# Kernel optimization log

Hardware: AMD Instinct MI355X
Metric: run time of the kernel (lower is better)

## Reference

```python
import jax, jax.numpy as jnp
import numpy as np

ED = 1024   # encoder_dim
GH = 1024   # gnn_hidden
NL = 3      # gnn_layers
NH = 8      # gnn_heads
HD = GH // NH
N = 2048    # graph nodes
B = 1024    # query/doc batch
TEMP = 0.05
LAPW = 0.1

def _layernorm(x, g, b):
    mu = jnp.mean(x, axis=-1, keepdims=True)
    var = jnp.mean((x - mu) ** 2, axis=-1, keepdims=True)
    return (x - mu) * jax.lax.rsqrt(var + 1e-5) * g + b

def _mlp_proj(x, W1, b1, g, beta, W2, b2):
    h = _layernorm(x @ W1 + b1, g, beta)
    h = jax.nn.gelu(h, approximate=False)
    return h @ W2 + b2

def _l2norm(x):
    n = jnp.linalg.norm(x, axis=-1, keepdims=True)
    return x / jnp.maximum(n, 1e-12)

def _gnn(x, adj, gatW, a1, a2, ln_g, ln_b, poW, pob):
    mask = adj > 0
    for l in range(NL):
        Wh = jnp.einsum('nf,hfo->hno', x, gatW[l])            # [H,N,HD]
        # a([Wh_i, Wh_j]) == Wh_i@a1 + Wh_j@a2 (linear, no bias): avoids NxNx2F concat
        s1 = jnp.einsum('hno,ho->hn', Wh, a1[l])
        s2 = jnp.einsum('hno,ho->hn', Wh, a2[l])
        e = jax.nn.leaky_relu(s1[:, :, None] + s2[:, None, :], 0.2)  # [H,N,N]
        att = jax.nn.softmax(jnp.where(mask[None], e, -9e15), axis=-1)
        h = jnp.einsum('hnm,hmo->hno', att, Wh)               # [H,N,HD]
        h = jnp.transpose(h, (1, 0, 2)).reshape(x.shape[0], GH)  # concat heads
        h = jax.nn.elu(_layernorm(h, ln_g[l], ln_b[l]))
        x = x + h  # in_features == hidden so residual applies every layer
    return x @ poW + pob

def _forward(query_embeds, pos_doc_embeds, node_embeds, adj, laplacian, params):
    (qW1, qb1, qg, qbt, qW2, qb2,
     dW1, db1, dg, dbt, dW2, db2,
     gatW, a1, a2, ln_g, ln_b, poW, pob) = params
    graph_embeds = _gnn(node_embeds, adj, gatW, a1, a2, ln_g, ln_b, poW, pob)
    q = _l2norm(_mlp_proj(query_embeds, qW1, qb1, qg, qbt, qW2, qb2))
    p = _l2norm(_mlp_proj(pos_doc_embeds, dW1, db1, dg, dbt, dW2, db2))
    pos_sim = jnp.sum(q * p, axis=-1) / TEMP                  # [B]
    neg_sim = (q @ p.T) / TEMP                                # [B,B]
    logits = jnp.concatenate([pos_sim[:, None], neg_sim], axis=1)
    info_nce = jnp.mean(jax.nn.logsumexp(logits, axis=-1) - logits[:, 0])
    lap = jnp.sum(graph_embeds * (laplacian @ graph_embeds)) / graph_embeds.shape[0]
    return info_nce + LAPW * lap, info_nce, lap

def setup_inputs() -> dict:
    key = jax.random.key(0)
    ks = jax.random.split(key, 24)
    r = lambda k, s: jax.random.normal(k, s, jnp.float32) * 0.02
    adj = (jax.random.uniform(ks[3], (N, N)) < 0.02).astype(jnp.float32)
    adj = jnp.maximum(adj, jnp.eye(N, dtype=jnp.float32))
    return {
        'query_embeds': jax.random.normal(ks[0], (B, ED), jnp.float32),
        'pos_doc_embeds': jax.random.normal(ks[1], (B, ED), jnp.float32),
        'node_embeds': jax.random.normal(ks[2], (N, ED), jnp.float32),
        'adj': adj,
        'laplacian': r(ks[4], (N, N)),
        'qW1': r(ks[5], (ED, ED)), 'qb1': jnp.zeros((ED,), jnp.float32),
        'qg': jnp.ones((ED,), jnp.float32), 'qbt': jnp.zeros((ED,), jnp.float32),
        'qW2': r(ks[6], (ED, ED)), 'qb2': jnp.zeros((ED,), jnp.float32),
        'dW1': r(ks[7], (ED, ED)), 'db1': jnp.zeros((ED,), jnp.float32),
        'dg': jnp.ones((ED,), jnp.float32), 'dbt': jnp.zeros((ED,), jnp.float32),
        'dW2': r(ks[8], (ED, ED)), 'db2': jnp.zeros((ED,), jnp.float32),
        'gatW': r(ks[9], (NL, NH, ED, HD)),
        'a1': r(ks[10], (NL, NH, HD)),
        'a2': r(ks[11], (NL, NH, HD)),
        'ln_g': jnp.ones((NL, GH), jnp.float32),
        'ln_b': jnp.zeros((NL, GH), jnp.float32),
        'poW': r(ks[12], (GH, ED)),
        'pob': jnp.zeros((ED,), jnp.float32),
    }

def reference(query_embeds, pos_doc_embeds, node_embeds, adj, laplacian,
              qW1, qb1, qg, qbt, qW2, qb2,
              dW1, db1, dg, dbt, dW2, db2,
              gatW, a1, a2, ln_g, ln_b, poW, pob):
    params = (qW1, qb1, qg, qbt, qW2, qb2,
              dW1, db1, dg, dbt, dW2, db2,
              gatW, a1, a2, ln_g, ln_b, poW, pob)
    return _forward(query_embeds, pos_doc_embeds, node_embeds, adj, laplacian, params)
```

## Files before the change

kernel.cpp:

```cpp
#include <hip/hip_runtime.h>
#include <math.h>

#define ED    1024
#define GH    1024
#define NLAY  3
#define NHEAD 8
#define HD    128
#define NNODE 2048
#define BQ    1024
#define CAP   192

typedef unsigned short u16;
typedef __attribute__((ext_vector_type(8))) short short8;
typedef __attribute__((ext_vector_type(4))) float f32x4;

static const size_t OFF_X    = 0;
static const size_t OFF_XB   = 2097152;
static const size_t OFF_WHB  = 3145728;
static const size_t OFF_WTG  = 4194304;
static const size_t OFF_WTPO = 5767168;
static const size_t OFF_WTQ1 = 6291456;
static const size_t OFF_WTD1 = 6815744;
static const size_t OFF_WTQ2 = 7340032;
static const size_t OFF_WTD2 = 7864320;
static const size_t OFF_G    = 8388608;
static const size_t OFF_GT   = 10485760;
static const size_t OFF_QPB  = 11534336;
static const size_t OFF_HF   = 12582912;
static const size_t OFF_HB   = 14680064;
static const size_t OFF_FF   = 15728640;
static const size_t OFF_FB   = 17825792;
static const size_t OFF_NEG  = 18874368;
static const size_t OFF_SV1  = 19922944;
static const size_t OFF_SV2  = 19939328;
static const size_t OFF_ACC  = 19955712;
static const size_t OFF_NCNT = 19955720;
static const size_t OFF_NBR  = 19957768;

__device__ __forceinline__ u16 f2bf(float f) {
  unsigned int u = __float_as_uint(f);
  return (u16)((u + 0x7fffu + ((u >> 16) & 1u)) >> 16);
}
__device__ __forceinline__ float bf2f(u16 u) {
  return __uint_as_float(((unsigned int)u) << 16);
}

__device__ __forceinline__ float waveSum(float v) {
#pragma unroll
  for (int off = 32; off; off >>= 1) v += __shfl_xor(v, off, 64);
  return v;
}
__device__ __forceinline__ float waveMax(float v) {
#pragma unroll
  for (int off = 32; off; off >>= 1) v = fmaxf(v, __shfl_xor(v, off, 64));
  return v;
}
__device__ __forceinline__ float blockSum(float v) {
  __shared__ float buf[4];
  int lane = threadIdx.x & 63, wid = threadIdx.x >> 6, nw = (blockDim.x + 63) >> 6;
  v = waveSum(v);
  __syncthreads();
  if (lane == 0) buf[wid] = v;
  __syncthreads();
  float r = buf[0];
  for (int i = 1; i < nw; ++i) r += buf[i];
  return r;
}
__device__ __forceinline__ float blockMax(float v) {
  __shared__ float buf[4];
  int lane = threadIdx.x & 63, wid = threadIdx.x >> 6, nw = (blockDim.x + 63) >> 6;
  v = waveMax(v);
  __syncthreads();
  if (lane == 0) buf[wid] = v;
  __syncthreads();
  float r = buf[0];
  for (int i = 1; i < nw; ++i) r = fmaxf(r, buf[i]);
  return r;
}

__global__ __launch_bounds__(256) void gemm128(
    const u16* __restrict__ A, const u16* __restrict__ B0,
    const u16* __restrict__ B1, float* __restrict__ C, u16* __restrict__ Cb,
    u16* __restrict__ Ct,
    const float* __restrict__ bias0, const float* __restrict__ bias1,
    int M, int N, int K, int split, float scale) {
  __shared__ u16 As[2][128][32];
  __shared__ u16 Bs[2][128][32];
  const int tid = threadIdx.x, wave = tid >> 6, lane = tid & 63;
  const int bm = blockIdx.y * 128, bn = blockIdx.x * 128;
  const u16* Bt = (bm < split) ? B0 : B1;
  const float* bias = (bm < split) ? bias0 : bias1;

  const int sr = tid >> 2, ss = tid & 3;
  const u16* ga0 = A  + (size_t)(bm + sr) * K + ss * 8;
  const u16* ga1 = A  + (size_t)(bm + sr + 64) * K + ss * 8;
  const u16* gb0 = Bt + (size_t)(bn + sr) * K + ss * 8;
  const u16* gb1 = Bt + (size_t)(bn + sr + 64) * K + ss * 8;

  const int r16 = lane & 15, kg = lane >> 4;
  const int wm = (wave >> 1) * 64, wn = (wave & 1) * 64;

  f32x4 acc[4][4] = {};
  const int nk = K >> 5;

  float4 pa0 = *(const float4*)ga0;
  float4 pa1 = *(const float4*)ga1;
  float4 pb0 = *(const float4*)gb0;
  float4 pb1 = *(const float4*)gb1;

  for (int kt = 0; kt < nk; ++kt) {
    const int p = kt & 1;
    *(float4*)&As[p][sr][ss * 8]      = pa0;
    *(float4*)&As[p][sr + 64][ss * 8] = pa1;
    *(float4*)&Bs[p][sr][ss * 8]      = pb0;
    *(float4*)&Bs[p][sr + 64][ss * 8] = pb1;
    __syncthreads();
    if (kt + 1 < nk) {
      ga0 += 32; ga1 += 32; gb0 += 32; gb1 += 32;
      pa0 = *(const float4*)ga0;
      pa1 = *(const float4*)ga1;
      pb0 = *(const float4*)gb0;
      pb1 = *(const float4*)gb1;
    }
    short8 av[4], bv[4];
#pragma unroll
    for (int i = 0; i < 4; ++i)
      av[i] = *(const short8*)&As[p][wm + i * 16 + r16][kg * 8];
#pragma unroll
    for (int j = 0; j < 4; ++j)
      bv[j] = *(const short8*)&Bs[p][wn + j * 16 + r16][kg * 8];
#pragma unroll
    for (int i = 0; i < 4; ++i)
#pragma unroll
      for (int j = 0; j < 4; ++j)
        acc[i][j] = __builtin_amdgcn_mfma_f32_16x16x32_bf16(av[i], bv[j], acc[i][j], 0, 0, 0);
  }

  if (C) {
#pragma unroll
    for (int j = 0; j < 4; ++j) {
      int col = bn + wn + j * 16 + r16;
      float bvv = bias ? bias[col] : 0.f;
#pragma unroll
      for (int i = 0; i < 4; ++i) {
        int row0 = bm + wm + i * 16 + kg * 4;
        float* cp = C + (size_t)row0 * N + col;
#pragma unroll
        for (int r = 0; r < 4; ++r)
          cp[(size_t)r * N] = acc[i][j][r] * scale + bvv;
      }
    }
  }
  if (Cb) {
#pragma unroll
    for (int j = 0; j < 4; ++j) {
      int col = bn + wn + j * 16 + r16;
      float bvv = bias ? bias[col] : 0.f;
#pragma unroll
      for (int i = 0; i < 4; ++i) {
        int row0 = bm + wm + i * 16 + kg * 4;
        u16* cp = Cb + (size_t)row0 * N + col;
#pragma unroll
        for (int r = 0; r < 4; ++r)
          cp[(size_t)r * N] = f2bf(acc[i][j][r] * scale + bvv);
      }
    }
  }
  if (Ct) {
#pragma unroll
    for (int j = 0; j < 4; ++j) {
      int col = bn + wn + j * 16 + r16;
      float bvv = bias ? bias[col] : 0.f;
#pragma unroll
      for (int i = 0; i < 4; ++i) {
        int row0 = bm + wm + i * 16 + kg * 4;
        ushort4 o;
        o.x = f2bf(acc[i][j][0] * scale + bvv);
        o.y = f2bf(acc[i][j][1] * scale + bvv);
        o.z = f2bf(acc[i][j][2] * scale + bvv);
        o.w = f2bf(acc[i][j][3] * scale + bvv);
        *(ushort4*)&Ct[(size_t)col * M + row0] = o;
      }
    }
  }
}

__global__ __launch_bounds__(256) void gemm_dual(
    const u16* __restrict__ A0, const u16* __restrict__ B00,
    const u16* __restrict__ B01, float* __restrict__ C0, u16* __restrict__ D0,
    const float* __restrict__ e0, const float* __restrict__ f0, int M0, int sp0, float sc0,
    const float* __restrict__ A1v, const float* __restrict__ A2v,
    float* __restrict__ S1o, float* __restrict__ S2o,
    const u16* __restrict__ A1, const u16* __restrict__ B10,
    const u16* __restrict__ B11, float* __restrict__ C1, u16* __restrict__ D1,
    const float* __restrict__ e1, const float* __restrict__ f1, int M1, int sp1, float sc1) {
  const int z = blockIdx.z;
  const u16* A   = z ? A1 : A0;
  const u16* Bt0 = z ? B10 : B00;
  const u16* Bt1 = z ? B11 : B01;
  float* C = z ? C1 : C0;
  u16*   D = z ? D1 : D0;
  const float* bias0 = z ? e1 : e0;
  const float* bias1 = z ? f1 : f0;
  const int M = z ? M1 : M0, split = z ? sp1 : sp0;
  const float scale = z ? sc1 : sc0;
  const int bm = blockIdx.y * 128, bn = blockIdx.x * 128;
  if (bm >= M) return;
  const int N = 1024, K = 1024;
  const u16* Bt = (bm < split) ? Bt0 : Bt1;
  const float* bias = (bm < split) ? bias0 : bias1;

  __shared__ u16 As[2][128][32];
  __shared__ u16 Bs[2][128][32];
  const int tid = threadIdx.x, wave = tid >> 6, lane = tid & 63;
  const int sr = tid >> 2, ss = tid & 3;
  const u16* ga0 = A  + (size_t)(bm + sr) * K + ss * 8;
  const u16* ga1 = A  + (size_t)(bm + sr + 64) * K + ss * 8;
  const u16* gb0 = Bt + (size_t)(bn + sr) * K + ss * 8;
  const u16* gb1 = Bt + (size_t)(bn + sr + 64) * K + ss * 8;
  const int r16 = lane & 15, kg = lane >> 4;
  const int wm = (wave >> 1) * 64, wn = (wave & 1) * 64;

  f32x4 acc[4][4] = {};
  const int nk = 32;

  float4 pa0 = *(const float4*)ga0;
  float4 pa1 = *(const float4*)ga1;
  float4 pb0 = *(const float4*)gb0;
  float4 pb1 = *(const float4*)gb1;

  for (int kt = 0; kt < nk; ++kt) {
    const int p = kt & 1;
    *(float4*)&As[p][sr][ss * 8]      = pa0;
    *(float4*)&As[p][sr + 64][ss * 8] = pa1;
    *(float4*)&Bs[p][sr][ss * 8]      = pb0;
    *(float4*)&Bs[p][sr + 64][ss * 8] = pb1;
    __syncthreads();
    if (kt + 1 < nk) {
      ga0 += 32; ga1 += 32; gb0 += 32; gb1 += 32;
      pa0 = *(const float4*)ga0;
      pa1 = *(const float4*)ga1;
      pb0 = *(const float4*)gb0;
      pb1 = *(const float4*)gb1;
    }
    short8 av[4], bv[4];
#pragma unroll
    for (int i = 0; i < 4; ++i)
      av[i] = *(const short8*)&As[p][wm + i * 16 + r16][kg * 8];
#pragma unroll
    for (int j = 0; j < 4; ++j)
      bv[j] = *(const short8*)&Bs[p][wn + j * 16 + r16][kg * 8];
#pragma unroll
    for (int i = 0; i < 4; ++i)
#pragma unroll
      for (int j = 0; j < 4; ++j)
        acc[i][j] = __builtin_amdgcn_mfma_f32_16x16x32_bf16(av[i], bv[j], acc[i][j], 0, 0, 0);
  }

  if (C) {
#pragma unroll
    for (int j = 0; j < 4; ++j) {
      int col = bn + wn + j * 16 + r16;
      float bvv = bias ? bias[col] : 0.f;
#pragma unroll
      for (int i = 0; i < 4; ++i) {
        int row0 = bm + wm + i * 16 + kg * 4;
        float* cp = C + (size_t)row0 * N + col;
#pragma unroll
        for (int r = 0; r < 4; ++r)
          cp[(size_t)r * N] = acc[i][j][r] * scale + bvv;
      }
    }
  }
  if (D) {
#pragma unroll
    for (int j = 0; j < 4; ++j) {
      int col = bn + wn + j * 16 + r16;
      float bvv = bias ? bias[col] : 0.f;
#pragma unroll
      for (int i = 0; i < 4; ++i) {
        int row0 = bm + wm + i * 16 + kg * 4;
        u16* cp = D + (size_t)row0 * N + col;
#pragma unroll
        for (int r = 0; r < 4; ++r)
          cp[(size_t)r * N] = f2bf(acc[i][j][r] * scale + bvv);
      }
    }
  }

  if (z == 0 && S1o) {
    float c1[4], c2[4];
#pragma unroll
    for (int j = 0; j < 4; ++j) {
      int col = bn + wn + j * 16 + r16;
      c1[j] = A1v[col]; c2[j] = A2v[col];
    }
    float r1[4][4], r2[4][4];
#pragma unroll
    for (int i = 0; i < 4; ++i)
#pragma unroll
      for (int r = 0; r < 4; ++r) {
        float v1 = 0.f, v2 = 0.f;
#pragma unroll
        for (int j = 0; j < 4; ++j) {
          v1 += acc[i][j][r] * c1[j];
          v2 += acc[i][j][r] * c2[j];
        }
#pragma unroll
        for (int off = 8; off; off >>= 1) {
          v1 += __shfl_xor(v1, off, 64);
          v2 += __shfl_xor(v2, off, 64);
        }
        r1[i][r] = v1; r2[i][r] = v2;
      }
    __syncthreads();
    float* sb1 = (float*)&As[0][0][0];
    float* sb2 = sb1 + 256;
    if (r16 == 0) {
      int half = wn >> 6;
#pragma unroll
      for (int i = 0; i < 4; ++i)
#pragma unroll
        for (int r = 0; r < 4; ++r) {
          int row = wm + i * 16 + kg * 4 + r;
          sb1[half * 128 + row] = r1[i][r];
          sb2[half * 128 + row] = r2[i][r];
        }
    }
    __syncthreads();
    if (tid < 128) {
      int h = blockIdx.x;
      S1o[(h << 11) + bm + tid] = sb1[tid] + sb1[128 + tid];
      S2o[(h << 11) + bm + tid] = sb2[tid] + sb2[128 + tid];
    }
  }
}

__global__ __launch_bounds__(256) void lap_gemm(
    const float* __restrict__ A, const u16* __restrict__ Bt,
    const float* __restrict__ G, float* __restrict__ acc_out) {
  __shared__ u16 As[2][128][32];
  __shared__ u16 Bs[2][128][32];
  const int tid = threadIdx.x, wave = tid >> 6, lane = tid & 63;
  const int n = blockIdx.x;
  const int member = n >> 6, gzy = n & 63;
  const int bm = (gzy & 15) * 128, bn = member * 128, k0 = (gzy >> 4) * 512;

  const int sr = tid >> 2, ss = tid & 3;
  const float* gA0 = A + (size_t)(bm + sr) * NNODE + k0 + ss * 8;
  const float* gA1 = gA0 + (size_t)64 * NNODE;
  const u16* gb0 = Bt + (size_t)(bn + sr) * NNODE + k0 + ss * 8;
  const u16* gb1 = Bt + (size_t)(bn + sr + 64) * NNODE + k0 + ss * 8;

  const int r16 = lane & 15, kg = lane >> 4;
  const int wm = (wave >> 1) * 64, wn = (wave & 1) * 64;

  f32x4 acc[4][4] = {};
  const int nk = 16;

  float4 a0l = *(const float4*)gA0, a0h = *(const float4*)(gA0 + 4);
  float4 a1l = *(const float4*)gA1, a1h = *(const float4*)(gA1 + 4);
  float4 pb0 = *(const float4*)gb0;
  float4 pb1 = *(const float4*)gb1;

  for (int kt = 0; kt < nk; ++kt) {
    const int p = kt & 1;
    {
      ushort4 lo, hi;
      lo.x = f2bf(a0l.x); lo.y = f2bf(a0l.y); lo.z = f2bf(a0l.z); lo.w = f2bf(a0l.w);
      hi.x = f2bf(a0h.x); hi.y = f2bf(a0h.y); hi.z = f2bf(a0h.z); hi.w = f2bf(a0h.w);
      *(ushort4*)&As[p][sr][ss * 8]     = lo;
      *(ushort4*)&As[p][sr][ss * 8 + 4] = hi;
      lo.x = f2bf(a1l.x); lo.y = f2bf(a1l.y); lo.z = f2bf(a1l.z); lo.w = f2bf(a1l.w);
      hi.x = f2bf(a1h.x); hi.y = f2bf(a1h.y); hi.z = f2bf(a1h.z); hi.w = f2bf(a1h.w);
      *(ushort4*)&As[p][sr + 64][ss * 8]     = lo;
      *(ushort4*)&As[p][sr + 64][ss * 8 + 4] = hi;
    }
    *(float4*)&Bs[p][sr][ss * 8]      = pb0;
    *(float4*)&Bs[p][sr + 64][ss * 8] = pb1;
    __syncthreads();
    if (kt + 1 < nk) {
      gA0 += 32; gA1 += 32; gb0 += 32; gb1 += 32;
      a0l = *(const float4*)gA0; a0h = *(const float4*)(gA0 + 4);
      a1l = *(const float4*)gA1; a1h = *(const float4*)(gA1 + 4);
      pb0 = *(const float4*)gb0;
      pb1 = *(const float4*)gb1;
    }
    short8 av[4], bv[4];
#pragma unroll
    for (int i = 0; i < 4; ++i)
      av[i] = *(const short8*)&As[p][wm + i * 16 + r16][kg * 8];
#pragma unroll
    for (int j = 0; j < 4; ++j)
      bv[j] = *(const short8*)&Bs[p][wn + j * 16 + r16][kg * 8];
#pragma unroll
    for (int i = 0; i < 4; ++i)
#pragma unroll
      for (int j = 0; j < 4; ++j)
        acc[i][j] = __builtin_amdgcn_mfma_f32_16x16x32_bf16(av[i], bv[j], acc[i][j], 0, 0, 0);
  }

  float sum = 0.f;
#pragma unroll
  for (int j = 0; j < 4; ++j) {
    int col = bn + wn + j * 16 + r16;
#pragma unroll
    for (int i = 0; i < 4; ++i) {
      int row0 = bm + wm + i * 16 + kg * 4;
      const float* gp = G + (size_t)row0 * ED + col;
#pragma unroll
      for (int r = 0; r < 4; ++r)
        sum += acc[i][j][r] * gp[(size_t)r * ED];
    }
  }
  sum = blockSum(sum);
  if (tid == 0) atomicAdd(acc_out, sum);
}

__global__ __launch_bounds__(256) void fused_att(
    const u16* __restrict__ WHb, const float* __restrict__ S1,
    const float* __restrict__ S2, const int* __restrict__ nbr,
    const int* __restrict__ ncnt, float* __restrict__ X, u16* __restrict__ Xb,
    const float* __restrict__ g, const float* __restrict__ b) {
  __shared__ int snb[CAP];
  __shared__ float pw[NHEAD][CAP];
  const int n = blockIdx.x, t = threadIdx.x;
  const int h = t >> 5, l = t & 31;
  const int cnt = ncnt[n];
  const int cntP = (cnt + 7) & ~7;
  for (int j = t; j < cnt; j += 256) snb[j] = nbr[n * CAP + j];
  __syncthreads();
  for (int j = cnt + t; j < cntP; j += 256) snb[j] = snb[0];

  const float s1v = S1[(h << 11) + n];
  float ev[6];
  float lmax = -1e30f;
  int ne = 0;
  for (int j = l; j < cnt; j += 32) {
    float e = s1v + S2[(h << 11) + snb[j]];
    e = e > 0.f ? e : 0.2f * e;
    ev[ne++] = e;
    lmax = fmaxf(lmax, e);
  }
#pragma unroll
  for (int off = 16; off; off >>= 1) lmax = fmaxf(lmax, __shfl_xor(lmax, off, 64));
  float lsum = 0.f;
  ne = 0;
  for (int j = l; j < cnt; j += 32) {
    float p = __expf(ev[ne++] - lmax);
    pw[h][j] = p;
    lsum += p;
  }
  for (int j = cnt + l; j < cntP; j += 32) pw[h][j] = 0.f;
#pragma unroll
  for (int off = 16; off; off >>= 1) lsum += __shfl_xor(lsum, off, 64);
  const float inv = 1.f / lsum;
  __syncthreads();

  float o0 = 0.f, o1 = 0.f, o2 = 0.f, o3 = 0.f;
  const u16* wp = WHb + (t << 2);
  for (int j0 = 0; j0 < cntP; j0 += 8) {
    ushort4 buf[8];
#pragma unroll
    for (int u = 0; u < 8; ++u)
      buf[u] = *(const ushort4*)(wp + ((size_t)snb[j0 + u] << 10));
#pragma unroll
    for (int u = 0; u < 8; ++u) {
      float w = pw[h][j0 + u];
      o0 += w * bf2f(buf[u].x);
      o1 += w * bf2f(buf[u].y);
      o2 += w * bf2f(buf[u].z);
      o3 += w * bf2f(buf[u].w);
    }
  }
  o0 *= inv; o1 *= inv; o2 *= inv; o3 *= inv;

  float s  = o0 + o1 + o2 + o3;
  float sq = o0 * o0 + o1 * o1 + o2 * o2 + o3 * o3;
  float mean = blockSum(s) * (1.f / 1024.f);
  float var  = blockSum(sq) * (1.f / 1024.f) - mean * mean;
  float rstd = rsqrtf(fmaxf(var, 0.f) + 1e-5f);
  float4 xv = *(float4*)&X[((size_t)n << 10) + (t << 2)];
  float ov[4] = {o0, o1, o2, o3};
  float xa[4] = {xv.x, xv.y, xv.z, xv.w};
#pragma unroll
  for (int i = 0; i < 4; ++i) {
    int c = (t << 2) + i;
    float y = (ov[i] - mean) * rstd * g[c] + b[c];
    y = y > 0.f ? y : expm1f(y);
    xa[i] += y;
  }
  *(float4*)&X[((size_t)n << 10) + (t << 2)] = make_float4(xa[0], xa[1], xa[2], xa[3]);
  ushort4 o;
  o.x = f2bf(xa[0]); o.y = f2bf(xa[1]); o.z = f2bf(xa[2]); o.w = f2bf(xa[3]);
  *(ushort4*)&Xb[((size_t)n << 10) + (t << 2)] = o;
}

__global__ void build_nbr(const float* __restrict__ adj, int* __restrict__ nbr,
                          int* __restrict__ ncnt, float* __restrict__ acc) {
  __shared__ int cnt;
  int n = blockIdx.x, tid = threadIdx.x;
  if (n == 0 && tid < 2) acc[tid] = 0.f;
  if (tid == 0) cnt = 0;
  __syncthreads();
  for (int c = tid; c < NNODE; c += 256) {
    if (adj[((size_t)n << 11) + c] > 0.f) {
      int p = atomicAdd(&cnt, 1);
      if (p < CAP) nbr[n * CAP + p] = c;
    }
  }
  __syncthreads();
  if (tid == 0) ncnt[n] = cnt < CAP ? cnt : CAP;
}

__global__ __launch_bounds__(256) void cvt_dual(const float* __restrict__ in,
                                                float* __restrict__ Xf,
                                                u16* __restrict__ Xb) {
  int i = blockIdx.x * 256 + threadIdx.x;
  float4 v = ((const float4*)in)[i];
  ((float4*)Xf)[i] = v;
  ushort4 o;
  o.x = f2bf(v.x); o.y = f2bf(v.y); o.z = f2bf(v.z); o.w = f2bf(v.w);
  ((ushort4*)Xb)[i] = o;
}

__global__ __launch_bounds__(256) void qd_cvt(const float* __restrict__ q,
                                              const float* __restrict__ d,
                                              u16* __restrict__ out) {
  int i = blockIdx.x * 256 + threadIdx.x;
  const int half = BQ * ED / 4;
  const float* src = (i < half) ? q : d;
  int j = (i < half) ? i : i - half;
  float4 v = ((const float4*)src)[j];
  ushort4 o;
  o.x = f2bf(v.x); o.y = f2bf(v.y); o.z = f2bf(v.z); o.w = f2bf(v.w);
  ((ushort4*)out)[i] = o;
}

__device__ __forceinline__ void cvt_tr_body(const float* ip, u16* op, int R, int C) {
  __shared__ float T[64][65];
  int r0 = blockIdx.y * 64, c0 = blockIdx.x * 64;
  int t = threadIdx.x;
#pragma unroll
  for (int p = 0; p < 4; ++p) {
    int row = p * 16 + (t >> 4), col = (t & 15) * 4;
    float4 v = *(const float4*)&ip[(size_t)(r0 + row) * C + c0 + col];
    T[row][col] = v.x; T[row][col + 1] = v.y;
    T[row][col + 2] = v.z; T[row][col + 3] = v.w;
  }
  __syncthreads();
#pragma unroll
  for (int p = 0; p < 4; ++p) {
    int c = p * 16 + (t >> 4), r = (t & 15) * 4;
    ushort4 o;
    o.x = f2bf(T[r][c]); o.y = f2bf(T[r + 1][c]);
    o.z = f2bf(T[r + 2][c]); o.w = f2bf(T[r + 3][c]);
    *(ushort4*)&op[(size_t)(c0 + c) * R + r0 + r] = o;
  }
}

__global__ __launch_bounds__(256) void cvt_transpose(
    const float* __restrict__ in, u16* __restrict__ out,
    int R, int C, long inb, long outb) {
  cvt_tr_body(in + (size_t)blockIdx.z * inb, out + (size_t)blockIdx.z * outb, R, C);
}

__global__ __launch_bounds__(256) void cvt_transpose5(
    const float* __restrict__ i0, u16* __restrict__ o0,
    const float* __restrict__ i1, u16* __restrict__ o1,
    const float* __restrict__ i2, u16* __restrict__ o2,
    const float* __restrict__ i3, u16* __restrict__ o3,
    const float* __restrict__ i4, u16* __restrict__ o4) {
  const float* in; u16* out;
  switch (blockIdx.z) {
    case 0: in = i0; out = o0; break;
    case 1: in = i1; out = o1; break;
    case 2: in = i2; out = o2; break;
    case 3: in = i3; out = o3; break;
    default: in = i4; out = o4; break;
  }
  cvt_tr_body(in, out, 1024, 1024);
}

__global__ __launch_bounds__(256) void ln_gelu(
    const float* __restrict__ IN, u16* __restrict__ OUT,
    const float* __restrict__ g0, const float* __restrict__ b0,
    const float* __restrict__ g1, const float* __restrict__ b1) {
  int row = blockIdx.x, tid = threadIdx.x;
  const float* g = (row < 1024) ? g0 : g1;
  const float* b = (row < 1024) ? b0 : b1;
  float4 v = *(const float4*)&IN[((size_t)row << 10) + (tid << 2)];
  float s = v.x + v.y + v.z + v.w;
  float sq = v.x * v.x + v.y * v.y + v.z * v.z + v.w * v.w;
  float mean = blockSum(s) * (1.f / 1024.f);
  float var = blockSum(sq) * (1.f / 1024.f) - mean * mean;
  float rstd = rsqrtf(fmaxf(var, 0.f) + 1e-5f);
  float vals[4] = {v.x, v.y, v.z, v.w};
  ushort4 o;
  u16* oa = (u16*)&o;
#pragma unroll
  for (int i = 0; i < 4; ++i) {
    int c = (tid << 2) + i;
    float y = (vals[i] - mean) * rstd * g[c] + b[c];
    y = 0.5f * y * (1.f + erff(y * 0.70710678118654752f));
    oa[i] = f2bf(y);
  }
  *(ushort4*)&OUT[((size_t)row << 10) + (tid << 2)] = o;
}

__global__ __launch_bounds__(256) void l2norm_k(const float* __restrict__ IN,
                                                u16* __restrict__ OUT) {
  int row = blockIdx.x, tid = threadIdx.x;
  float4 v = *(const float4*)&IN[((size_t)row << 10) + (tid << 2)];
  float sq = v.x * v.x + v.y * v.y + v.z * v.z + v.w * v.w;
  float s = blockSum(sq);
  float inv = 1.f / fmaxf(sqrtf(s), 1e-12f);
  ushort4 o;
  o.x = f2bf(v.x * inv); o.y = f2bf(v.y * inv);
  o.z = f2bf(v.z * inv); o.w = f2bf(v.w * inv);
  *(ushort4*)&OUT[((size_t)row << 10) + (tid << 2)] = o;
}

__global__ __launch_bounds__(256) void lse_kernel(const float* __restrict__ NEG,
                                                  float* __restrict__ acc) {
  int bq = blockIdx.x, tid = threadIdx.x;
  const float* row = NEG + ((size_t)bq << 10);
  float4 v = *(const float4*)&row[tid << 2];
  float lm = fmaxf(fmaxf(v.x, v.y), fmaxf(v.z, v.w));
  float m = blockMax(lm);
  float ls = __expf(v.x - m) + __expf(v.y - m) + __expf(v.z - m) + __expf(v.w - m);
  float ssum = blockSum(ls);
  if (tid == 0) {
    float pos = row[bq];
    float loss = m + logf(ssum + __expf(pos - m)) - pos;
    atomicAdd(acc + 1, loss);
  }
}

__global__ void final_kernel(const float* __restrict__ acc, float* __restrict__ out) {
  float lap = acc[0] / 2048.f;
  float info = acc[1] / 1024.f;
  out[0] = info + 0.1f * lap;
  out[1] = info;
  out[2] = lap;
}

extern "C" void kernel_launch(void* const* d_in, const int* in_sizes, int n_in,
                              void* d_out, int out_size, void* d_ws, size_t ws_size,
                              hipStream_t stream) {
  const float* query = (const float*)d_in[0];
  const float* docs  = (const float*)d_in[1];
  const float* nodes = (const float*)d_in[2];
  const float* adj   = (const float*)d_in[3];
  const float* lapl  = (const float*)d_in[4];
  const float* qW1 = (const float*)d_in[5],  *qb1 = (const float*)d_in[6];
  const float* qg  = (const float*)d_in[7],  *qbt = (const float*)d_in[8];
  const float* qW2 = (const float*)d_in[9],  *qb2 = (const float*)d_in[10];
  const float* dW1 = (const float*)d_in[11], *db1 = (const float*)d_in[12];
  const float* dg  = (const float*)d_in[13], *dbt = (const float*)d_in[14];
  const float* dW2 = (const float*)d_in[15], *db2 = (const float*)d_in[16];
  const float* gatW = (const float*)d_in[17];
  const float* a1   = (const float*)d_in[18];
  const float* a2   = (const float*)d_in[19];
  const float* ln_g = (const float*)d_in[20];
  const float* ln_b = (const float*)d_in[21];
  const float* poW  = (const float*)d_in[22];
  const float* pob  = (const float*)d_in[23];
  float* out = (float*)d_out;

  float* ws = (float*)d_ws;
  float* X    = ws + OFF_X;
  u16*   Xb   = (u16*)(ws + OFF_XB);
  u16*   WHb  = (u16*)(ws + OFF_WHB);
  u16*   WtG  = (u16*)(ws + OFF_WTG);
  u16*   WtPO = (u16*)(ws + OFF_WTPO);
  u16*   WtQ1 = (u16*)(ws + OFF_WTQ1);
  u16*   WtD1 = (u16*)(ws + OFF_WTD1);
  u16*   WtQ2 = (u16*)(ws + OFF_WTQ2);
  u16*   WtD2 = (u16*)(ws + OFF_WTD2);
  float* G    = ws + OFF_G;
  u16*   Gt   = (u16*)(ws + OFF_GT);
  u16*   QPb  = (u16*)(ws + OFF_QPB);
  float* Hf   = ws + OFF_HF;
  u16*   Hb   = (u16*)(ws + OFF_HB);
  float* Ff   = ws + OFF_FF;
  u16*   Fb   = (u16*)(ws + OFF_FB);
  float* NEG  = ws + OFF_NEG;
  float* S1v  = ws + OFF_SV1;
  float* S2v  = ws + OFF_SV2;
  float* ACC  = ws + OFF_ACC;
  int*   NCNT = (int*)(ws + OFF_NCNT);
  int*   NBR  = (int*)(ws + OFF_NBR);

  const size_t WSL = (size_t)GH * ED;

  build_nbr<<<NNODE, 256, 0, stream>>>(adj, NBR, NCNT, ACC);
  cvt_dual<<<2048, 256, 0, stream>>>(nodes, X, Xb);
  qd_cvt<<<2048, 256, 0, stream>>>(query, docs, QPb);
  cvt_transpose<<<dim3(2, 16, 24), 256, 0, stream>>>(
      gatW, WtG, ED, HD, (long)ED * HD, (long)HD * ED);
  cvt_transpose5<<<dim3(16, 16, 5), 256, 0, stream>>>(
      poW, WtPO, qW1, WtQ1, dW1, WtD1, qW2, WtQ2, dW2, WtD2);

  gemm_dual<<<dim3(8, 16, 2), 256, 0, stream>>>(
      Xb, WtG, WtG, nullptr, WHb, nullptr, nullptr, NNODE, NNODE, 1.f,
      a1, a2, S1v, S2v,
      QPb, WtQ1, WtD1, Hf, nullptr, qb1, db1, 2 * BQ, BQ, 1.f);
  fused_att<<<NNODE, 256, 0, stream>>>(WHb, S1v, S2v, NBR, NCNT, X, Xb, ln_g, ln_b);
  ln_gelu<<<2 * BQ, 256, 0, stream>>>(Hf, Hb, qg, qbt, dg, dbt);

  gemm_dual<<<dim3(8, 16, 2), 256, 0, stream>>>(
      Xb, WtG + WSL, WtG + WSL, nullptr, WHb, nullptr, nullptr, NNODE, NNODE, 1.f,
      a1 + NHEAD * HD, a2 + NHEAD * HD, S1v, S2v,
      Hb, WtQ2, WtD2, Ff, nullptr, qb2, db2, 2 * BQ, BQ, 1.f);
  fused_att<<<NNODE, 256, 0, stream>>>(WHb, S1v, S2v, NBR, NCNT, X, Xb,
      ln_g + GH, ln_b + GH);
  l2norm_k<<<2 * BQ, 256, 0, stream>>>(Ff, Fb);

  gemm_dual<<<dim3(8, 16, 2), 256, 0, stream>>>(
      Xb, WtG + 2 * WSL, WtG + 2 * WSL, nullptr, WHb, nullptr, nullptr, NNODE, NNODE, 1.f,
      a1 + 2 * NHEAD * HD, a2 + 2 * NHEAD * HD, S1v, S2v,
      Fb, Fb + (size_t)BQ * ED, Fb + (size_t)BQ * ED, NEG, nullptr,
      nullptr, nullptr, BQ, BQ, 20.f);
  fused_att<<<NNODE, 256, 0, stream>>>(WHb, S1v, S2v, NBR, NCNT, X, Xb,
      ln_g + 2 * GH, ln_b + 2 * GH);
  lse_kernel<<<BQ, 256, 0, stream>>>(NEG, ACC);

  gemm128<<<dim3(ED / 128, NNODE / 128), 256, 0, stream>>>(
      Xb, WtPO, WtPO, G, nullptr, Gt, pob, pob, NNODE, ED, GH, NNODE, 1.f);
  lap_gemm<<<512, 256, 0, stream>>>(lapl, Gt, G, ACC);

  final_kernel<<<1, 1, 0, stream>>>(ACC, out);
}
```

Baseline: 381.8 us.

## Merge small kernels into fused launches and finalize in last lap_gemm block

Combines the three prep kernels into one grid, folds ln_gelu, l2norm and logsumexp work into the attention kernel as extra blocks, and drops the final kernel by letting the last lap_gemm block write outputs via an atomic counter. lap_gemm split-K is doubled (1024 blocks, K=256 each), the attention gather unroll goes from 8 to 16, and the A-tile store is widened to one 16-byte write. The aim is fewer launches and better overlap between independent small ops, at the cost of more atomics and register pressure.

After: 386.2 us. About the same (+1.1%).

```diff
diff --git a/kernel.cpp b/kernel.cpp
--- a/kernel.cpp
+++ b/kernel.cpp
@@ -9,6 +9,7 @@
 #define NNODE 2048
 #define BQ    1024
 #define CAP   192
+#define CAPP  208
 
 typedef unsigned short u16;
 typedef __attribute__((ext_vector_type(8))) short short8;
@@ -34,6 +35,7 @@
 static const size_t OFF_SV1  = 19922944;
 static const size_t OFF_SV2  = 19939328;
 static const size_t OFF_ACC  = 19955712;
+static const size_t OFF_CNT  = 19955714;
 static const size_t OFF_NCNT = 19955720;
 static const size_t OFF_NBR  = 19957768;
 
@@ -338,13 +340,14 @@
 
 __global__ __launch_bounds__(256) void lap_gemm(
     const float* __restrict__ A, const u16* __restrict__ Bt,
-    const float* __restrict__ G, float* __restrict__ acc_out) {
+    const float* __restrict__ G, float* __restrict__ acc,
+    int* __restrict__ cnt_done, float* __restrict__ out) {
   __shared__ u16 As[2][128][32];
   __shared__ u16 Bs[2][128][32];
   const int tid = threadIdx.x, wave = tid >> 6, lane = tid & 63;
   const int n = blockIdx.x;
-  const int member = n >> 6, gzy = n & 63;
-  const int bm = (gzy & 15) * 128, bn = member * 128, k0 = (gzy >> 4) * 512;
+  const int bn = (n >> 7) * 128, strip = n & 127;
+  const int bm = (strip & 15) * 128, k0 = (strip >> 4) * 256;
 
   const int sr = tid >> 2, ss = tid & 3;
   const float* gA0 = A + (size_t)(bm + sr) * NNODE + k0 + ss * 8;
@@ -355,8 +358,8 @@
   const int r16 = lane & 15, kg = lane >> 4;
   const int wm = (wave >> 1) * 64, wn = (wave & 1) * 64;
 
-  f32x4 acc[4][4] = {};
-  const int nk = 16;
+  f32x4 acc_r[4][4] = {};
+  const int nk = 8;
 
   float4 a0l = *(const float4*)gA0, a0h = *(const float4*)(gA0 + 4);
   float4 a1l = *(const float4*)gA1, a1h = *(const float4*)(gA1 + 4);
@@ -366,15 +369,17 @@
   for (int kt = 0; kt < nk; ++kt) {
     const int p = kt & 1;
     {
-      ushort4 lo, hi;
-      lo.x = f2bf(a0l.x); lo.y = f2bf(a0l.y); lo.z = f2bf(a0l.z); lo.w = f2bf(a0l.w);
-      hi.x = f2bf(a0h.x); hi.y = f2bf(a0h.y); hi.z = f2bf(a0h.z); hi.w = f2bf(a0h.w);
-      *(ushort4*)&As[p][sr][ss * 8]     = lo;
-      *(ushort4*)&As[p][sr][ss * 8 + 4] = hi;
-      lo.x = f2bf(a1l.x); lo.y = f2bf(a1l.y); lo.z = f2bf(a1l.z); lo.w = f2bf(a1l.w);
-      hi.x = f2bf(a1h.x); hi.y = f2bf(a1h.y); hi.z = f2bf(a1h.z); hi.w = f2bf(a1h.w);
-      *(ushort4*)&As[p][sr + 64][ss * 8]     = lo;
-      *(ushort4*)&As[p][sr + 64][ss * 8 + 4] = hi;
+      union { short8 v; ushort4 u4[2]; } w;
+      w.u4[0].x = f2bf(a0l.x); w.u4[0].y = f2bf(a0l.y);
+      w.u4[0].z = f2bf(a0l.z); w.u4[0].w = f2bf(a0l.w);
+      w.u4[1].x = f2bf(a0h.x); w.u4[1].y = f2bf(a0h.y);
+      w.u4[1].z = f2bf(a0h.z); w.u4[1].w = f2bf(a0h.w);
+      *(short8*)&As[p][sr][ss * 8] = w.v;
+      w.u4[0].x = f2bf(a1l.x); w.u4[0].y = f2bf(a1l.y);
+      w.u4[0].z = f2bf(a1l.z); w.u4[0].w = f2bf(a1l.w);
+      w.u4[1].x = f2bf(a1h.x); w.u4[1].y = f2bf(a1h.y);
+      w.u4[1].z = f2bf(a1h.z); w.u4[1].w = f2bf(a1h.w);
+      *(short8*)&As[p][sr + 64][ss * 8] = w.v;
     }
     *(float4*)&Bs[p][sr][ss * 8]      = pb0;
     *(float4*)&Bs[p][sr + 64][ss * 8] = pb1;
@@ -397,7 +402,7 @@
     for (int i = 0; i < 4; ++i)
 #pragma unroll
       for (int j = 0; j < 4; ++j)
-        acc[i][j] = __builtin_amdgcn_mfma_f32_16x16x32_bf16(av[i], bv[j], acc[i][j], 0, 0, 0);
+        acc_r[i][j] = __builtin_amdgcn_mfma_f32_16x16x32_bf16(av[i], bv[j], acc_r[i][j], 0, 0, 0);
   }
 
   float sum = 0.f;
@@ -410,131 +415,191 @@
       const float* gp = G + (size_t)row0 * ED + col;
 #pragma unroll
       for (int r = 0; r < 4; ++r)
-        sum += acc[i][j][r] * gp[(size_t)r * ED];
+        sum += acc_r[i][j][r] * gp[(size_t)r * ED];
     }
   }
   sum = blockSum(sum);
-  if (tid == 0) atomicAdd(acc_out, sum);
-}
-
-__global__ __launch_bounds__(256) void fused_att(
+  if (tid == 0) {
+    atomicAdd(acc, sum);
+    __threadfence();
+    int prev = atomicAdd(cnt_done, 1);
+    if (prev == (int)gridDim.x - 1) {
+      float lap  = atomicAdd(acc, 0.f) / 2048.f;
+      float info = atomicAdd(acc + 1, 0.f) / 1024.f;
+      out[0] = info + 0.1f * lap;
+      out[1] = info;
+      out[2] = lap;
+    }
+  }
+}
+
+__global__ __launch_bounds__(256) void att_elem(
     const u16* __restrict__ WHb, const float* __restrict__ S1,
     const float* __restrict__ S2, const int* __restrict__ nbr,
     const int* __restrict__ ncnt, float* __restrict__ X, u16* __restrict__ Xb,
-    const float* __restrict__ g, const float* __restrict__ b) {
-  __shared__ int snb[CAP];
-  __shared__ float pw[NHEAD][CAP];
-  const int n = blockIdx.x, t = threadIdx.x;
-  const int h = t >> 5, l = t & 31;
-  const int cnt = ncnt[n];
-  const int cntP = (cnt + 7) & ~7;
-  for (int j = t; j < cnt; j += 256) snb[j] = nbr[n * CAP + j];
-  __syncthreads();
-  for (int j = cnt + t; j < cntP; j += 256) snb[j] = snb[0];
-
-  const float s1v = S1[(h << 11) + n];
-  float ev[6];
-  float lmax = -1e30f;
-  int ne = 0;
-  for (int j = l; j < cnt; j += 32) {
-    float e = s1v + S2[(h << 11) + snb[j]];
-    e = e > 0.f ? e : 0.2f * e;
-    ev[ne++] = e;
-    lmax = fmaxf(lmax, e);
-  }
-#pragma unroll
-  for (int off = 16; off; off >>= 1) lmax = fmaxf(lmax, __shfl_xor(lmax, off, 64));
-  float lsum = 0.f;
-  ne = 0;
-  for (int j = l; j < cnt; j += 32) {
-    float p = __expf(ev[ne++] - lmax);
-    pw[h][j] = p;
-    lsum += p;
-  }
-  for (int j = cnt + l; j < cntP; j += 32) pw[h][j] = 0.f;
-#pragma unroll
-  for (int off = 16; off; off >>= 1) lsum += __shfl_xor(lsum, off, 64);
-  const float inv = 1.f / lsum;
-  __syncthreads();
-
-  float o0 = 0.f, o1 = 0.f, o2 = 0.f, o3 = 0.f;
-  const u16* wp = WHb + (t << 2);
-  for (int j0 = 0; j0 < cntP; j0 += 8) {
-    ushort4 buf[8];
-#pragma unroll
-    for (int u = 0; u < 8; ++u)
-      buf[u] = *(const ushort4*)(wp + ((size_t)snb[j0 + u] << 10));
-#pragma unroll
-    for (int u = 0; u < 8; ++u) {
-      float w = pw[h][j0 + u];
-      o0 += w * bf2f(buf[u].x);
-      o1 += w * bf2f(buf[u].y);
-      o2 += w * bf2f(buf[u].z);
-      o3 += w * bf2f(buf[u].w);
-    }
-  }
-  o0 *= inv; o1 *= inv; o2 *= inv; o3 *= inv;
-
-  float s  = o0 + o1 + o2 + o3;
-  float sq = o0 * o0 + o1 * o1 + o2 * o2 + o3 * o3;
-  float mean = blockSum(s) * (1.f / 1024.f);
-  float var  = blockSum(sq) * (1.f / 1024.f) - mean * mean;
-  float rstd = rsqrtf(fmaxf(var, 0.f) + 1e-5f);
-  float4 xv = *(float4*)&X[((size_t)n << 10) + (t << 2)];
-  float ov[4] = {o0, o1, o2, o3};
-  float xa[4] = {xv.x, xv.y, xv.z, xv.w};
-#pragma unroll
-  for (int i = 0; i < 4; ++i) {
-    int c = (t << 2) + i;
-    float y = (ov[i] - mean) * rstd * g[c] + b[c];
-    y = y > 0.f ? y : expm1f(y);
-    xa[i] += y;
-  }
-  *(float4*)&X[((size_t)n << 10) + (t << 2)] = make_float4(xa[0], xa[1], xa[2], xa[3]);
-  ushort4 o;
-  o.x = f2bf(xa[0]); o.y = f2bf(xa[1]); o.z = f2bf(xa[2]); o.w = f2bf(xa[3]);
-  *(ushort4*)&Xb[((size_t)n << 10) + (t << 2)] = o;
-}
-
-__global__ void build_nbr(const float* __restrict__ adj, int* __restrict__ nbr,
-                          int* __restrict__ ncnt, float* __restrict__ acc) {
-  __shared__ int cnt;
-  int n = blockIdx.x, tid = threadIdx.x;
-  if (n == 0 && tid < 2) acc[tid] = 0.f;
-  if (tid == 0) cnt = 0;
-  __syncthreads();
-  for (int c = tid; c < NNODE; c += 256) {
-    if (adj[((size_t)n << 11) + c] > 0.f) {
-      int p = atomicAdd(&cnt, 1);
-      if (p < CAP) nbr[n * CAP + p] = c;
-    }
-  }
-  __syncthreads();
-  if (tid == 0) ncnt[n] = cnt < CAP ? cnt : CAP;
-}
-
-__global__ __launch_bounds__(256) void cvt_dual(const float* __restrict__ in,
-                                                float* __restrict__ Xf,
-                                                u16* __restrict__ Xb) {
-  int i = blockIdx.x * 256 + threadIdx.x;
-  float4 v = ((const float4*)in)[i];
-  ((float4*)Xf)[i] = v;
-  ushort4 o;
-  o.x = f2bf(v.x); o.y = f2bf(v.y); o.z = f2bf(v.z); o.w = f2bf(v.w);
-  ((ushort4*)Xb)[i] = o;
-}
-
-__global__ __launch_bounds__(256) void qd_cvt(const float* __restrict__ q,
-                                              const float* __restrict__ d,
-                                              u16* __restrict__ out) {
-  int i = blockIdx.x * 256 + threadIdx.x;
-  const int half = BQ * ED / 4;
-  const float* src = (i < half) ? q : d;
-  int j = (i < half) ? i : i - half;
-  float4 v = ((const float4*)src)[j];
-  ushort4 o;
-  o.x = f2bf(v.x); o.y = f2bf(v.y); o.z = f2bf(v.z); o.w = f2bf(v.w);
-  ((ushort4*)out)[i] = o;
+    const float* __restrict__ g, const float* __restrict__ b,
+    int mode, const float* __restrict__ EIN, u16* __restrict__ EOUT,
+    const float* __restrict__ g0, const float* __restrict__ b0,
+    const float* __restrict__ g1, const float* __restrict__ b1,
+    float* __restrict__ acc) {
+  const int t = threadIdx.x;
+  if (blockIdx.x < NNODE) {
+    __shared__ int snb[CAPP];
+    __shared__ float pw[NHEAD][CAPP];
+    const int n = blockIdx.x;
+    const int h = t >> 5, l = t & 31;
+    const int cnt = ncnt[n];
+    const int cntP = (cnt + 15) & ~15;
+    for (int j = t; j < cnt; j += 256) snb[j] = nbr[n * CAP + j];
+    __syncthreads();
+    for (int j = cnt + t; j < cntP; j += 256) snb[j] = snb[0];
+
+    const float s1v = S1[(h << 11) + n];
+    float ev[6];
+    float lmax = -1e30f;
+    int ne = 0;
+    for (int j = l; j < cnt; j += 32) {
+      float e = s1v + S2[(h << 11) + snb[j]];
+      e = e > 0.f ? e : 0.2f * e;
+      ev[ne++] = e;
+      lmax = fmaxf(lmax, e);
+    }
+#pragma unroll
+    for (int off = 16; off; off >>= 1) lmax = fmaxf(lmax, __shfl_xor(lmax, off, 64));
+    float lsum = 0.f;
+    ne = 0;
+    for (int j = l; j < cnt; j += 32) {
+      float p = __expf(ev[ne++] - lmax);
+      pw[h][j] = p;
+      lsum += p;
+    }
+    for (int j = cnt + l; j < cntP; j += 32) pw[h][j] = 0.f;
+#pragma unroll
+    for (int off = 16; off; off >>= 1) lsum += __shfl_xor(lsum, off, 64);
+    const float inv = 1.f / lsum;
+    __syncthreads();
+
+    float o0 = 0.f, o1 = 0.f, o2 = 0.f, o3 = 0.f;
+    const u16* wp = WHb + (t << 2);
+    for (int j0 = 0; j0 < cntP; j0 += 16) {
+      ushort4 buf[16];
+#pragma unroll
+      for (int u = 0; u < 16; ++u)
+        buf[u] = *(const ushort4*)(wp + ((size_t)snb[j0 + u] << 10));
+#pragma unroll
+      for (int u = 0; u < 16; ++u) {
+        float w = pw[h][j0 + u];
+        o0 += w * bf2f(buf[u].x);
+        o1 += w * bf2f(buf[u].y);
+        o2 += w * bf2f(buf[u].z);
+        o3 += w * bf2f(buf[u].w);
+      }
+    }
+    o0 *= inv; o1 *= inv; o2 *= inv; o3 *= inv;
+
+    float s  = o0 + o1 + o2 + o3;
+    float sq = o0 * o0 + o1 * o1 + o2 * o2 + o3 * o3;
+    float mean = blockSum(s) * (1.f / 1024.f);
+    float var  = blockSum(sq) * (1.f / 1024.f) - mean * mean;
+    float rstd = rsqrtf(fmaxf(var, 0.f) + 1e-5f);
+    float4 xv = *(float4*)&X[((size_t)n << 10) + (t << 2)];
+    float ov[4] = {o0, o1, o2, o3};
+    float xa[4] = {xv.x, xv.y, xv.z, xv.w};
+#pragma unroll
+    for (int i = 0; i < 4; ++i) {
+      int c = (t << 2) + i;
+      float y = (ov[i] - mean) * rstd * g[c] + b[c];
+      y = y > 0.f ? y : expm1f(y);
+      xa[i] += y;
+    }
+    *(float4*)&X[((size_t)n << 10) + (t << 2)] = make_float4(xa[0], xa[1], xa[2], xa[3]);
+    ushort4 o;
+    o.x = f2bf(xa[0]); o.y = f2bf(xa[1]); o.z = f2bf(xa[2]); o.w = f2bf(xa[3]);
+    *(ushort4*)&Xb[((size_t)n << 10) + (t << 2)] = o;
+  } else {
+    const int row = blockIdx.x - NNODE;
+    if (mode == 0) {
+      const float* gg = (row < 1024) ? g0 : g1;
+      const float* bb = (row < 1024) ? b0 : b1;
+      float4 v = *(const float4*)&EIN[((size_t)row << 10) + (t << 2)];
+      float s = v.x + v.y + v.z + v.w;
+      float sq = v.x * v.x + v.y * v.y + v.z * v.z + v.w * v.w;
+      float mean = blockSum(s) * (1.f / 1024.f);
+      float var = blockSum(sq) * (1.f / 1024.f) - mean * mean;
+      float rstd = rsqrtf(fmaxf(var, 0.f) + 1e-5f);
+      float vals[4] = {v.x, v.y, v.z, v.w};
+      ushort4 o;
+      u16* oa = (u16*)&o;
+#pragma unroll
+      for (int i = 0; i < 4; ++i) {
+        int c = (t << 2) + i;
+        float y = (vals[i] - mean) * rstd * gg[c] + bb[c];
+        y = 0.5f * y * (1.f + erff(y * 0.70710678118654752f));
+        oa[i] = f2bf(y);
+      }
+      *(ushort4*)&EOUT[((size_t)row << 10) + (t << 2)] = o;
+    } else if (mode == 1) {
+      float4 v = *(const float4*)&EIN[((size_t)row << 10) + (t << 2)];
+      float sq = v.x * v.x + v.y * v.y + v.z * v.z + v.w * v.w;
+      float s = blockSum(sq);
+      float inv = 1.f / fmaxf(sqrtf(s), 1e-12f);
+      ushort4 o;
+      o.x = f2bf(v.x * inv); o.y = f2bf(v.y * inv);
+      o.z = f2bf(v.z * inv); o.w = f2bf(v.w * inv);
+      *(ushort4*)&EOUT[((size_t)row << 10) + (t << 2)] = o;
+    } else {
+      const float* rw = EIN + ((size_t)row << 10);
+      float4 v = *(const float4*)&rw[t << 2];
+      float lm = fmaxf(fmaxf(v.x, v.y), fmaxf(v.z, v.w));
+      float m = blockMax(lm);
+      float ls = __expf(v.x - m) + __expf(v.y - m) + __expf(v.z - m) + __expf(v.w - m);
+      float ssum = blockSum(ls);
+      if (t == 0) {
+        float pos = rw[row];
+        float loss = m + logf(ssum + __expf(pos - m)) - pos;
+        atomicAdd(acc + 1, loss);
+      }
+    }
+  }
+}
+
+__global__ __launch_bounds__(256) void prep_mega(
+    const float* __restrict__ adj, int* __restrict__ nbr, int* __restrict__ ncnt,
+    float* __restrict__ acc, int* __restrict__ cnt_done,
+    const float* __restrict__ nodes, float* __restrict__ Xf, u16* __restrict__ Xb,
+    const float* __restrict__ q, const float* __restrict__ d, u16* __restrict__ QPb) {
+  const int bx = blockIdx.x, tid = threadIdx.x;
+  if (bx < NNODE) {
+    __shared__ int cnt;
+    if (bx == 0 && tid < 2) acc[tid] = 0.f;
+    if (bx == 0 && tid == 2) *cnt_done = 0;
+    if (tid == 0) cnt = 0;
+    __syncthreads();
+    for (int c = tid; c < NNODE; c += 256) {
+      if (adj[((size_t)bx << 11) + c] > 0.f) {
+        int p = atomicAdd(&cnt, 1);
+        if (p < CAP) nbr[bx * CAP + p] = c;
+      }
+    }
+    __syncthreads();
+    if (tid == 0) ncnt[bx] = cnt < CAP ? cnt : CAP;
+  } else if (bx < 2 * NNODE) {
+    int i = (bx - NNODE) * 256 + tid;
+    float4 v = ((const float4*)nodes)[i];
+    ((float4*)Xf)[i] = v;
+    ushort4 o;
+    o.x = f2bf(v.x); o.y = f2bf(v.y); o.z = f2bf(v.z); o.w = f2bf(v.w);
+    ((ushort4*)Xb)[i] = o;
+  } else {
+    int i = (bx - 2 * NNODE) * 256 + tid;
+    const int half = BQ * ED / 4;
+    const float* src = (i < half) ? q : d;
+    int j = (i < half) ? i : i - half;
+    float4 v = ((const float4*)src)[j];
+    ushort4 o;
+    o.x = f2bf(v.x); o.y = f2bf(v.y); o.z = f2bf(v.z); o.w = f2bf(v.w);
+    ((ushort4*)QPb)[i] = o;
+  }
 }
 
 __device__ __forceinline__ void cvt_tr_body(const float* ip, u16* op, int R, int C) {
@@ -580,69 +645,6 @@
     default: in = i4; out = o4; break;
   }
   cvt_tr_body(in, out, 1024, 1024);
-}
-
-__global__ __launch_bounds__(256) void ln_gelu(
-    const float* __restrict__ IN, u16* __restrict__ OUT,
-    const float* __restrict__ g0, const float* __restrict__ b0,
-    const float* __restrict__ g1, const float* __restrict__ b1) {
-  int row = blockIdx.x, tid = threadIdx.x;
-  const float* g = (row < 1024) ? g0 : g1;
-  const float* b = (row < 1024) ? b0 : b1;
-  float4 v = *(const float4*)&IN[((size_t)row << 10) + (tid << 2)];
-  float s = v.x + v.y + v.z + v.w;
-  float sq = v.x * v.x + v.y * v.y + v.z * v.z + v.w * v.w;
-  float mean = blockSum(s) * (1.f / 1024.f);
-  float var = blockSum(sq) * (1.f / 1024.f) - mean * mean;
-  float rstd = rsqrtf(fmaxf(var, 0.f) + 1e-5f);
-  float vals[4] = {v.x, v.y, v.z, v.w};
-  ushort4 o;
-  u16* oa = (u16*)&o;
-#pragma unroll
-  for (int i = 0; i < 4; ++i) {
-    int c = (tid << 2) + i;
-    float y = (vals[i] - mean) * rstd * g[c] + b[c];
-    y = 0.5f * y * (1.f + erff(y * 0.70710678118654752f));
-    oa[i] = f2bf(y);
-  }
-  *(ushort4*)&OUT[((size_t)row << 10) + (tid << 2)] = o;
-}
-
-__global__ __launch_bounds__(256) void l2norm_k(const float* __restrict__ IN,
-                                                u16* __restrict__ OUT) {
-  int row = blockIdx.x, tid = threadIdx.x;
-  float4 v = *(const float4*)&IN[((size_t)row << 10) + (tid << 2)];
-  float sq = v.x * v.x + v.y * v.y + v.z * v.z + v.w * v.w;
-  float s = blockSum(sq);
-  float inv = 1.f / fmaxf(sqrtf(s), 1e-12f);
-  ushort4 o;
-  o.x = f2bf(v.x * inv); o.y = f2bf(v.y * inv);
-  o.z = f2bf(v.z * inv); o.w = f2bf(v.w * inv);
-  *(ushort4*)&OUT[((size_t)row << 10) + (tid << 2)] = o;
-}
-
-__global__ __launch_bounds__(256) void lse_kernel(const float* __restrict__ NEG,
-                                                  float* __restrict__ acc) {
-  int bq = blockIdx.x, tid = threadIdx.x;
-  const float* row = NEG + ((size_t)bq << 10);
-  float4 v = *(const float4*)&row[tid << 2];
-  float lm = fmaxf(fmaxf(v.x, v.y), fmaxf(v.z, v.w));
-  float m = blockMax(lm);
-  float ls = __expf(v.x - m) + __expf(v.y - m) + __expf(v.z - m) + __expf(v.w - m);
-  float ssum = blockSum(ls);
-  if (tid == 0) {
-    float pos = row[bq];
-    float loss = m + logf(ssum + __expf(pos - m)) - pos;
-    atomicAdd(acc + 1, loss);
-  }
-}
-
-__global__ void final_kernel(const float* __restrict__ acc, float* __restrict__ out) {
-  float lap = acc[0] / 2048.f;
-  float info = acc[1] / 1024.f;
-  out[0] = info + 0.1f * lap;
-  out[1] = info;
-  out[2] = lap;
 }
 
 extern "C" void kernel_launch(void* const* d_in, const int* in_sizes, int n_in,
@@ -689,14 +691,14 @@
   float* S1v  = ws + OFF_SV1;
   float* S2v  = ws + OFF_SV2;
   float* ACC  = ws + OFF_ACC;
+  int*   CNTD = (int*)(ws + OFF_CNT);
   int*   NCNT = (int*)(ws + OFF_NCNT);
   int*   NBR  = (int*)(ws + OFF_NBR);
 
   const size_t WSL = (size_t)GH * ED;
 
-  build_nbr<<<NNODE, 256, 0, stream>>>(adj, NBR, NCNT, ACC);
-  cvt_dual<<<2048, 256, 0, stream>>>(nodes, X, Xb);
-  qd_cvt<<<2048, 256, 0, stream>>>(query, docs, QPb);
+  prep_mega<<<3 * NNODE, 256, 0, stream>>>(
+      adj, NBR, NCNT, ACC, CNTD, nodes, X, Xb, query, docs, QPb);
   cvt_transpose<<<dim3(2, 16, 24), 256, 0, stream>>>(
       gatW, WtG, ED, HD, (long)ED * HD, (long)HD * ED);
   cvt_transpose5<<<dim3(16, 16, 5), 256, 0, stream>>>(
@@ -706,29 +708,28 @@
       Xb, WtG, WtG, nullptr, WHb, nullptr, nullptr, NNODE, NNODE, 1.f,
       a1, a2, S1v, S2v,
       QPb, WtQ1, WtD1, Hf, nullptr, qb1, db1, 2 * BQ, BQ, 1.f);
-  fused_att<<<NNODE, 256, 0, stream>>>(WHb, S1v, S2v, NBR, NCNT, X, Xb, ln_g, ln_b);
-  ln_gelu<<<2 * BQ, 256, 0, stream>>>(Hf, Hb, qg, qbt, dg, dbt);
+  att_elem<<<NNODE + 2 * BQ, 256, 0, stream>>>(
+      WHb, S1v, S2v, NBR, NCNT, X, Xb, ln_g, ln_b,
+      0, Hf, Hb, qg, qbt, dg, dbt, ACC);
 
   gemm_dual<<<dim3(8, 16, 2), 256, 0, stream>>>(
       Xb, WtG + WSL, WtG + WSL, nullptr, WHb, nullptr, nullptr, NNODE, NNODE, 1.f,
       a1 + NHEAD * HD, a2 + NHEAD * HD, S1v, S2v,
       Hb, WtQ2, WtD2, Ff, nullptr, qb2, db2, 2 * BQ, BQ, 1.f);
-  fused_att<<<NNODE, 256, 0, stream>>>(WHb, S1v, S2v, NBR, NCNT, X, Xb,
-      ln_g + GH, ln_b + GH);
-  l2norm_k<<<2 * BQ, 256, 0, stream>>>(Ff, Fb);
+  att_elem<<<NNODE + 2 * BQ, 256, 0, stream>>>(
+      WHb, S1v, S2v, NBR, NCNT, X, Xb, ln_g + GH, ln_b + GH,
+      1, Ff, Fb, nullptr, nullptr, nullptr, nullptr, ACC);
 
   gemm_dual<<<dim3(8, 16, 2), 256, 0, stream>>>(
       Xb, WtG + 2 * WSL, WtG + 2 * WSL, nullptr, WHb, nullptr, nullptr, NNODE, NNODE, 1.f,
       a1 + 2 * NHEAD * HD, a2 + 2 * NHEAD * HD, S1v, S2v,
       Fb, Fb + (size_t)BQ * ED, Fb + (size_t)BQ * ED, NEG, nullptr,
       nullptr, nullptr, BQ, BQ, 20.f);
-  fused_att<<<NNODE, 256, 0, stream>>>(WHb, S1v, S2v, NBR, NCNT, X, Xb,
-      ln_g + 2 * GH, ln_b + 2 * GH);
-  lse_kernel<<<BQ, 256, 0, stream>>>(NEG, ACC);
+  att_elem<<<NNODE + BQ, 256, 0, stream>>>(
+      WHb, S1v, S2v, NBR, NCNT, X, Xb, ln_g + 2 * GH, ln_b + 2 * GH,
+      2, NEG, nullptr, nullptr, nullptr, nullptr, nullptr, ACC);
 
   gemm128<<<dim3(ED / 128, NNODE / 128), 256, 0, stream>>>(
       Xb, WtPO, WtPO, G, nullptr, Gt, pob, pob, NNODE, ED, GH, NNODE, 1.f);
-  lap_gemm<<<512, 256, 0, stream>>>(lapl, Gt, G, ACC);
-
-  final_kernel<<<1, 1, 0, stream>>>(ACC, out);
-}
+  lap_gemm<<<1024, 256, 0, stream>>>(lapl, Gt, G, ACC, CNTD, out);
+}
```
